# Performance work log

Measured on AMD Instinct MI355X. Metric: run time of the kernel, lower is better.

Reference implementation:

```python
import jax, jax.numpy as jnp
import numpy as np

EPS = 1e-6
BETA = 0.25
NVQ_W = 1.0


def _mlp(h, params):
    # Linear + ReLU on all but last layer (dropout=0, bn=False)
    n = len(params)
    for i, (w, b) in enumerate(params):
        h = h @ w + b
        if i < n - 1:
            h = jax.nn.relu(h)
    return h


def _kuma_ab(a_raw, b_raw):
    return jax.nn.softplus(a_raw) + EPS, jax.nn.softplus(b_raw) + EPS


def _kuma_h(z, a, b):
    x = jnp.clip(jax.nn.sigmoid(z), EPS, 1.0 - EPS)
    inner = jnp.clip(1.0 - x ** a, EPS, 1.0)
    y = 1.0 - inner ** b
    return jnp.clip(y, EPS, 1.0 - EPS)


def _kuma_h_inv(y, a, b):
    y = jnp.clip(y, EPS, 1.0 - EPS)
    omy = jnp.clip(1.0 - y, EPS, 1.0)
    inner = jnp.clip(1.0 - omy ** (1.0 / b), EPS, 1.0 - EPS)
    x = jnp.clip(inner ** (1.0 / a), EPS, 1.0 - EPS)
    return jnp.log(x / (1.0 - x))


def _rq(z, codebooks):
    # Residual VQ: per level, squared-L2 nearest code (argmin), straight-through,
    # codebook + beta*commitment loss. sk_epsilon=0 -> Sinkhorn skipped.
    sg = jax.lax.stop_gradient
    residual = z
    x_q = jnp.zeros_like(z)
    losses, idx_list = [], []
    for l in range(codebooks.shape[0]):
        cb = codebooks[l]  # [K, D]
        d = (jnp.sum(residual * residual, -1, keepdims=True)
             + jnp.sum(cb * cb, -1)
             - 2.0 * residual @ cb.T)  # [B, K]
        idx = jnp.argmin(d, axis=-1)  # [B]
        q = cb[idx]  # [B, D]
        codebook_loss = jnp.mean((q - sg(residual)) ** 2)
        commit_loss = jnp.mean((sg(q) - residual) ** 2)
        losses.append(codebook_loss + BETA * commit_loss)
        q_st = residual + sg(q - residual)  # straight-through
        residual = residual - q_st
        x_q = x_q + q_st
        idx_list.append(idx)
    return x_q, jnp.mean(jnp.stack(losses)), jnp.stack(idx_list, axis=-1)


def _forward(x, enc, dec, codebooks, a_raw, b_raw):
    z = _mlp(x, enc)
    a, b = _kuma_ab(a_raw, b_raw)
    z_prime = _kuma_h(z, a, b)
    zq_prime, rq_loss, indices = _rq(z_prime, codebooks)
    z_q = _kuma_h_inv(zq_prime, a, b)
    z_recon = _kuma_h_inv(z_prime, a, b)
    nvq_loss = jnp.mean((z_recon - z) ** 2)
    total_quant_loss = rq_loss + NVQ_W * nvq_loss
    out = _mlp(z_q, dec)
    return out, total_quant_loss, indices


def setup_inputs() -> dict:
    key = jax.random.key(0)
    ks = jax.random.split(key, 16)
    B, IN = 16384, 768
    enc_dims = [768, 2048, 1024, 512, 128]
    dec_dims = enc_dims[::-1]

    def lin(k, din, dout):
        w = jax.random.normal(k, (din, dout), jnp.float32) * (1.0 / np.sqrt(din))
        return w, jnp.zeros((dout,), jnp.float32)

    inp = {"x": jax.random.normal(ks[0], (B, IN), jnp.float32)}
    for i in range(4):
        w, b = lin(ks[1 + i], enc_dims[i], enc_dims[i + 1])
        inp[f"enc_w{i}"], inp[f"enc_b{i}"] = w, b
        w, b = lin(ks[5 + i], dec_dims[i], dec_dims[i + 1])
        inp[f"dec_w{i}"], inp[f"dec_b{i}"] = w, b
    inp["codebooks"] = jax.random.normal(ks[9], (4, 256, 128), jnp.float32)
    inp["a_raw"] = jnp.zeros((128,), jnp.float32)
    inp["b_raw"] = jnp.zeros((128,), jnp.float32)
    return inp


def reference(x, enc_w0, enc_b0, enc_w1, enc_b1, enc_w2, enc_b2, enc_w3, enc_b3,
              dec_w0, dec_b0, dec_w1, dec_b1, dec_w2, dec_b2, dec_w3, dec_b3,
              codebooks, a_raw, b_raw):
    enc = [(enc_w0, enc_b0), (enc_w1, enc_b1), (enc_w2, enc_b2), (enc_w3, enc_b3)]
    dec = [(dec_w0, dec_b0), (dec_w1, dec_b1), (dec_w2, dec_b2), (dec_w3, dec_b3)]
    return _forward(x, enc, dec, codebooks, a_raw, b_raw)
```

## Files before the change

### kernel.cpp

```cpp
#include <hip/hip_runtime.h>
#include <math.h>

#define EPS_F 1e-6f
#define ONE_M_EPS (1.0f - 1e-6f)

typedef __attribute__((ext_vector_type(8))) short s16x8;
typedef __attribute__((ext_vector_type(8))) _Float16 f16x8;
typedef __attribute__((ext_vector_type(4))) float f32x4;

__device__ __forceinline__ ushort f2bf(float f) {
    union { float f; unsigned u; } v; v.f = f;
    unsigned u = v.u;
    return (ushort)((u + 0x7FFFu + ((u >> 16) & 1u)) >> 16);
}
__device__ __forceinline__ float bf2f(ushort h) {
    union { unsigned u; float f; } v; v.u = ((unsigned)h) << 16;
    return v.f;
}
__device__ __forceinline__ void split2h(float x, ushort& h, ushort& m) {
    union { _Float16 f; ushort u; } a, b;
    a.f = (_Float16)x;
    float r = x - (float)a.f;
    b.f = (_Float16)r;
    h = a.u; m = b.u;
}

#define GLL16(srcp, dstp)                                                     \
    __builtin_amdgcn_global_load_lds(                                         \
        (const __attribute__((address_space(1))) void*)(srcp),                \
        (__attribute__((address_space(3))) void*)(dstp), 16, 0, 0)

__device__ __forceinline__ int swz_k(int row, int k) { return k ^ ((row >> 1) & 3); }

template<bool RELU, int OUT2>
__global__ __launch_bounds__(256) void gemm_mfma_split2(
    const ushort* __restrict__ Ah, const ushort* __restrict__ Am,
    const ushort* __restrict__ Wh, const ushort* __restrict__ Wm,
    const float* __restrict__ bias,
    void* __restrict__ C0, void* __restrict__ C1,
    int M, int N, int K)
{
    __shared__ __align__(16) ushort As[2][128 * 32];
    __shared__ __align__(16) ushort Bs[2][128 * 32];

    const int tid  = threadIdx.x;
    const int lane = tid & 63;
    const int w    = tid >> 6;
    const int wm   = (w >> 1) * 64;
    const int wn   = (w & 1) * 64;
    const int bm   = blockIdx.x * 128;
    const int bn   = blockIdx.y * 128;

    f32x4 acc[4][4];
#pragma unroll
    for (int i = 0; i < 4; i++)
#pragma unroll
        for (int j = 0; j < 4; j++) acc[i][j] = f32x4{0.f, 0.f, 0.f, 0.f};

    const int c0 = (w * 2) * 64 + lane;
    const int c1 = (w * 2 + 1) * 64 + lane;
    const int r0 = c0 >> 2, k0e = swz_k(r0, c0 & 3) * 8;
    const int r1 = c1 >> 2, k1e = swz_k(r1, c1 & 3) * 8;

    const size_t a_off0 = (size_t)(bm + r0) * K + k0e;
    const size_t a_off1 = (size_t)(bm + r1) * K + k1e;
    const size_t b_off0 = (size_t)(bn + r0) * K + k0e;
    const size_t b_off1 = (size_t)(bn + r1) * K + k1e;
    const int d0 = (w * 2) * 512;
    const int d1 = (w * 2 + 1) * 512;

    const ushort* Ap[2] = {Ah, Am};
    const ushort* Wp[2] = {Wh, Wm};

    const int fm  = lane & 15;
    const int fkb = lane >> 4;

    for (int k0 = 0; k0 < K; k0 += 32) {
#pragma unroll
        for (int p = 0; p < 2; p++) {
            GLL16(Ap[p] + a_off0 + k0, &As[p][d0]);
            GLL16(Ap[p] + a_off1 + k0, &As[p][d1]);
            GLL16(Wp[p] + b_off0 + k0, &Bs[p][d0]);
            GLL16(Wp[p] + b_off1 + k0, &Bs[p][d1]);
        }
        __syncthreads();

        f16x8 af[2][4];
#pragma unroll
        for (int p = 0; p < 2; p++)
#pragma unroll
            for (int i = 0; i < 4; i++) {
                const int row = wm + i * 16 + fm;
                af[p][i] = *reinterpret_cast<const f16x8*>(
                    &As[p][row * 32 + swz_k(row, fkb) * 8]);
            }

#pragma unroll
        for (int q = 0; q < 2; q++) {
            f16x8 bq[4];
#pragma unroll
            for (int j = 0; j < 4; j++) {
                const int row = wn + j * 16 + fm;
                bq[j] = *reinterpret_cast<const f16x8*>(
                    &Bs[q][row * 32 + swz_k(row, fkb) * 8]);
            }
#pragma unroll
            for (int p = 0; p < 2; p++) {
                if (p + q <= 1) {
#pragma unroll
                    for (int i = 0; i < 4; i++)
#pragma unroll
                        for (int j = 0; j < 4; j++)
                            acc[i][j] = __builtin_amdgcn_mfma_f32_16x16x32_f16(
                                af[p][i], bq[j], acc[i][j], 0, 0, 0);
                }
            }
        }
        __syncthreads();
    }

#pragma unroll
    for (int j = 0; j < 4; j++) {
        const int coln = bn + wn + j * 16 + fm;
        const float bv = bias[coln];
#pragma unroll
        for (int i = 0; i < 4; i++) {
            const int row0 = bm + wm + i * 16 + (lane >> 4) * 4;
#pragma unroll
            for (int r = 0; r < 4; r++) {
                float o = acc[i][j][r] + bv;
                if (RELU) o = fmaxf(o, 0.f);
                const size_t idx = (size_t)(row0 + r) * N + coln;
                if (OUT2) {
                    ushort h, m;
                    split2h(o, h, m);
                    ((ushort*)C0)[idx] = h;
                    ((ushort*)C1)[idx] = m;
                } else {
                    ((float*)C0)[idx] = o;
                }
            }
        }
    }
}

template<bool RELU, bool OUT_BF16>
__global__ __launch_bounds__(256) void gemm_mfma_bt(
    const ushort* __restrict__ A, const ushort* __restrict__ WT,
    const float* __restrict__ bias, void* __restrict__ Cv,
    int M, int N, int K)
{
    __shared__ __align__(16) ushort As[128 * 32];
    __shared__ __align__(16) ushort Bs[128 * 32];

    const int tid  = threadIdx.x;
    const int lane = tid & 63;
    const int w    = tid >> 6;
    const int wm   = (w >> 1) * 64;
    const int wn   = (w & 1) * 64;
    const int bm   = blockIdx.x * 128;
    const int bn   = blockIdx.y * 128;

    f32x4 acc[4][4];
#pragma unroll
    for (int i = 0; i < 4; i++)
#pragma unroll
        for (int j = 0; j < 4; j++) acc[i][j] = f32x4{0.f, 0.f, 0.f, 0.f};

    const int c0 = (w * 2) * 64 + lane;
    const int c1 = (w * 2 + 1) * 64 + lane;
    const int r0 = c0 >> 2, k0e = swz_k(r0, c0 & 3) * 8;
    const int r1 = c1 >> 2, k1e = swz_k(r1, c1 & 3) * 8;

    const ushort* a_src0 = A  + (size_t)(bm + r0) * K + k0e;
    const ushort* a_src1 = A  + (size_t)(bm + r1) * K + k1e;
    const ushort* b_src0 = WT + (size_t)(bn + r0) * K + k0e;
    const ushort* b_src1 = WT + (size_t)(bn + r1) * K + k1e;
    ushort* a_dst0 = &As[(w * 2) * 512];
    ushort* a_dst1 = &As[(w * 2 + 1) * 512];
    ushort* b_dst0 = &Bs[(w * 2) * 512];
    ushort* b_dst1 = &Bs[(w * 2 + 1) * 512];

    const int fm  = lane & 15;
    const int fkb = lane >> 4;

    for (int k0 = 0; k0 < K; k0 += 32) {
        GLL16(a_src0 + k0, a_dst0);
        GLL16(a_src1 + k0, a_dst1);
        GLL16(b_src0 + k0, b_dst0);
        GLL16(b_src1 + k0, b_dst1);
        __syncthreads();

        s16x8 af[4], bfr[4];
#pragma unroll
        for (int i = 0; i < 4; i++) {
            const int row = wm + i * 16 + fm;
            af[i] = *reinterpret_cast<const s16x8*>(&As[row * 32 + swz_k(row, fkb) * 8]);
        }
#pragma unroll
        for (int j = 0; j < 4; j++) {
            const int row = wn + j * 16 + fm;
            bfr[j] = *reinterpret_cast<const s16x8*>(&Bs[row * 32 + swz_k(row, fkb) * 8]);
        }
#pragma unroll
        for (int i = 0; i < 4; i++)
#pragma unroll
            for (int j = 0; j < 4; j++)
                acc[i][j] = __builtin_amdgcn_mfma_f32_16x16x32_bf16(
                    af[i], bfr[j], acc[i][j], 0, 0, 0);
        __syncthreads();
    }

#pragma unroll
    for (int j = 0; j < 4; j++) {
        const int coln = bn + wn + j * 16 + fm;
        const float bv = bias[coln];
#pragma unroll
        for (int i = 0; i < 4; i++) {
            const int row0 = bm + wm + i * 16 + (lane >> 4) * 4;
#pragma unroll
            for (int r = 0; r < 4; r++) {
                float o = acc[i][j][r] + bv;
                if (RELU) o = fmaxf(o, 0.f);
                if (OUT_BF16)
                    ((ushort*)Cv)[(size_t)(row0 + r) * N + coln] = f2bf(o);
                else
                    ((float*)Cv)[(size_t)(row0 + r) * N + coln] = o;
            }
        }
    }
}

__global__ __launch_bounds__(256) void transpose_to_bf16(
    const float* __restrict__ W, ushort* __restrict__ WT, int K, int N)
{
    __shared__ float t[32][33];
    const int kb = blockIdx.x * 32, nb = blockIdx.y * 32;
    const int tx = threadIdx.x & 31, ty = threadIdx.x >> 5;
#pragma unroll
    for (int i = ty; i < 32; i += 8)
        t[i][tx] = W[(size_t)(kb + i) * N + nb + tx];
    __syncthreads();
#pragma unroll
    for (int i = ty; i < 32; i += 8)
        WT[(size_t)(nb + i) * K + kb + tx] = f2bf(t[tx][i]);
}

__global__ __launch_bounds__(256) void transpose_split_f16(
    const float* __restrict__ W, ushort* __restrict__ TH,
    ushort* __restrict__ TM, int K, int N)
{
    __shared__ float t[32][33];
    const int kb = blockIdx.x * 32, nb = blockIdx.y * 32;
    const int tx = threadIdx.x & 31, ty = threadIdx.x >> 5;
#pragma unroll
    for (int i = ty; i < 32; i += 8)
        t[i][tx] = W[(size_t)(kb + i) * N + nb + tx];
    __syncthreads();
#pragma unroll
    for (int i = ty; i < 32; i += 8) {
        ushort h, m;
        split2h(t[tx][i], h, m);
        const size_t idx = (size_t)(nb + i) * K + kb + tx;
        TH[idx] = h; TM[idx] = m;
    }
}

__global__ __launch_bounds__(256) void split_plane2_kernel(
    const float* __restrict__ X, ushort* __restrict__ H,
    ushort* __restrict__ M, size_t n)
{
    size_t i = (size_t)blockIdx.x * 256 + threadIdx.x;
    if (i >= n) return;
    ushort h, m;
    split2h(X[i], h, m);
    H[i] = h; M[i] = m;
}

__global__ __launch_bounds__(128) void prep_cb_kernel(
    const float* __restrict__ cb, float* __restrict__ cbT, float* __restrict__ cnorm)
{
    int b = blockIdx.x;
    int d = threadIdx.x;
    float v = cb[(size_t)b * 128 + d];
    int l = b >> 8, c = b & 255;
    cbT[((size_t)l * 128 + d) * 256 + c] = v;
    float s = v * v;
#pragma unroll
    for (int off = 32; off > 0; off >>= 1) s += __shfl_down(s, off);
    __shared__ float ps[2];
    if ((d & 63) == 0) ps[d >> 6] = s;
    __syncthreads();
    if (d == 0) cnorm[b] = ps[0] + ps[1];
}

__device__ __forceinline__ float softplusf(float x) {
    return (x > 20.f) ? x : log1pf(expf(x));
}

__global__ void kuma_ab_init(const float* __restrict__ a_raw, const float* __restrict__ b_raw,
                             float* __restrict__ kp)
{
    int t = threadIdx.x;
    if (t < 128) {
        float a = softplusf(a_raw[t]) + EPS_F;
        float b = softplusf(b_raw[t]) + EPS_F;
        kp[t] = a;
        kp[128 + t] = b;
        kp[256 + t] = 1.f / a;
        kp[384 + t] = 1.f / b;
    }
}

__global__ __launch_bounds__(256) void kuma_h_kernel(
    const float* __restrict__ z, const float* __restrict__ kp,
    float* __restrict__ zp, int n)
{
    int i = blockIdx.x * 256 + threadIdx.x;
    if (i >= n) return;
    int col = i & 127;
    float a = kp[col], b = kp[128 + col];
    float zv = z[i];
    float x = 1.f / (1.f + expf(-zv));
    x = fminf(fmaxf(x, EPS_F), ONE_M_EPS);
    float inner = 1.f - powf(x, a);
    inner = fminf(fmaxf(inner, EPS_F), 1.f);
    float y = 1.f - powf(inner, b);
    y = fminf(fmaxf(y, EPS_F), ONE_M_EPS);
    zp[i] = y;
}

__global__ __launch_bounds__(64) void rq_kernel2(
    const float* __restrict__ zp, const float* __restrict__ cb,
    const float* __restrict__ cbT, const float* __restrict__ cnorm,
    float* __restrict__ xq, float* __restrict__ idx_out,
    float* __restrict__ prq, int bid0, int nRq)
{
    __shared__ float res[4][128];

    const int t = threadIdx.x;
    const int row0 = blockIdx.x * 4;

#pragma unroll
    for (int j = 0; j < 8; j++) {
        int e = t + j * 64;
        res[e >> 7][e & 127] = zp[(size_t)row0 * 128 + e];
    }

    float lsum[4];

#pragma unroll 1
    for (int l = 0; l < 4; l++) {
        const float* cT = cbT + (size_t)l * 32768;

        float acc[4][4];
#pragma unroll
        for (int r = 0; r < 4; r++)
#pragma unroll
            for (int cc = 0; cc < 4; cc++) acc[r][cc] = 0.f;

        float pc[16];
#pragma unroll
        for (int dd = 0; dd < 4; dd++)
#pragma unroll
            for (int cc = 0; cc < 4; cc++)
                pc[dd * 4 + cc] = cT[dd * 256 + cc * 64 + t];

#pragma unroll 2
        for (int d = 0; d < 128; d += 4) {
            float nc[16];
            if (d < 124) {
#pragma unroll
                for (int dd = 0; dd < 4; dd++)
#pragma unroll
                    for (int cc = 0; cc < 4; cc++)
                        nc[dd * 4 + cc] = cT[(d + 4 + dd) * 256 + cc * 64 + t];
            }
#pragma unroll
            for (int r = 0; r < 4; r++) {
                float4 rv = *reinterpret_cast<const float4*>(&res[r][d]);
#pragma unroll
                for (int cc = 0; cc < 4; cc++) {
                    acc[r][cc] += rv.x * pc[cc] + rv.y * pc[4 + cc]
                                + rv.z * pc[8 + cc] + rv.w * pc[12 + cc];
                }
            }
#pragma unroll
            for (int k = 0; k < 16; k++) pc[k] = nc[k];
        }

        float cn[4];
#pragma unroll
        for (int cc = 0; cc < 4; cc++) cn[cc] = cnorm[l * 256 + cc * 64 + t];

        int bidx0, bidx1, bidx2, bidx3;
#pragma unroll
        for (int r = 0; r < 4; r++) {
            float dmin = cn[0] - 2.f * acc[r][0];
            int imin = t;
#pragma unroll
            for (int cc = 1; cc < 4; cc++) {
                float dv = cn[cc] - 2.f * acc[r][cc];
                if (dv < dmin) { dmin = dv; imin = cc * 64 + t; }
            }
#pragma unroll
            for (int off = 1; off < 64; off <<= 1) {
                float d2 = __shfl_xor(dmin, off);
                int i2 = __shfl_xor(imin, off);
                if (d2 < dmin || (d2 == dmin && i2 < imin)) { dmin = d2; imin = i2; }
            }
            if (r == 0) bidx0 = imin;
            else if (r == 1) bidx1 = imin;
            else if (r == 2) bidx2 = imin;
            else bidx3 = imin;
            if (t == 0) idx_out[(size_t)(row0 + r) * 4 + l] = (float)imin;
        }

        float s = 0.f;
#pragma unroll
        for (int j = 0; j < 8; j++) {
            const int r = j >> 1;
            const int d = (j & 1) * 64 + t;
            const int bi = (r == 0) ? bidx0 : (r == 1) ? bidx1 : (r == 2) ? bidx2 : bidx3;
            float q = cb[((size_t)(l * 256) + bi) * 128 + d];
            float nr = res[r][d] - q;
            res[r][d] = nr;
            s += nr * nr;
        }
        lsum[l] = s;
    }

#pragma unroll
    for (int j = 0; j < 8; j++) {
        int e = t + j * 64;
        xq[(size_t)row0 * 128 + e] = zp[(size_t)row0 * 128 + e] - res[e >> 7][e & 127];
    }

#pragma unroll
    for (int l = 0; l < 4; l++) {
        float s = lsum[l];
#pragma unroll
        for (int off = 32; off > 0; off >>= 1) s += __shfl_down(s, off);
        if (t == 0) prq[(size_t)l * nRq + bid0 + blockIdx.x] = s;
    }
}

__device__ __forceinline__ float kuma_h_inv_f(float y, float ia, float ib) {
    y = fminf(fmaxf(y, EPS_F), ONE_M_EPS);
    float omy = fminf(fmaxf(1.f - y, EPS_F), 1.f);
    float inner = fminf(fmaxf(1.f - powf(omy, ib), EPS_F), ONE_M_EPS);
    float x = fminf(fmaxf(powf(inner, ia), EPS_F), ONE_M_EPS);
    return logf(x / (1.f - x));
}

__global__ __launch_bounds__(256) void zq_nvq_kernel(
    const float* __restrict__ xq, const float* __restrict__ zp,
    const float* __restrict__ z, const float* __restrict__ kp,
    float* __restrict__ zq, ushort* __restrict__ zq16,
    float* __restrict__ pnvq, int bid0, int n)
{
    int i = blockIdx.x * 256 + threadIdx.x;
    float ds = 0.f;
    if (i < n) {
        int col = i & 127;
        float ia = kp[256 + col], ib = kp[384 + col];
        float xv = xq[i];
        float zpv = zp[i];
        float zv = z[i];
        float zr = kuma_h_inv_f(zpv, ia, ib);
        float d = zr - zv;
        ds = d * d;
        float zqv = kuma_h_inv_f(xv, ia, ib);
        zq[i] = zqv;
        zq16[i] = f2bf(zqv);
    }
#pragma unroll
    for (int off = 32; off > 0; off >>= 1) ds += __shfl_down(ds, off);
    __shared__ float ps[4];
    if ((threadIdx.x & 63) == 0) ps[threadIdx.x >> 6] = ds;
    __syncthreads();
    if (threadIdx.x == 0)
        pnvq[bid0 + blockIdx.x] = ps[0] + ps[1] + ps[2] + ps[3];
}

__global__ __launch_bounds__(256) void finalize_kernel(
    const float* __restrict__ prq, const float* __restrict__ pnvq,
    int nRqAll, int nNvq, float* __restrict__ out_loss)
{
    const int t = threadIdx.x;
    float srq = 0.f, snvq = 0.f;
    for (int i = t; i < nRqAll; i += 256) srq += prq[i];
    for (int i = t; i < nNvq; i += 256) snvq += pnvq[i];
#pragma unroll
    for (int off = 32; off > 0; off >>= 1) {
        srq += __shfl_down(srq, off);
        snvq += __shfl_down(snvq, off);
    }
    __shared__ float pr[4], pn[4];
    if ((t & 63) == 0) { pr[t >> 6] = srq; pn[t >> 6] = snvq; }
    __syncthreads();
    if (t == 0) {
        const float inv = 1.f / (16384.f * 128.f);
        float rq = (pr[0] + pr[1] + pr[2] + pr[3]);
        float nv = (pn[0] + pn[1] + pn[2] + pn[3]);
        out_loss[0] = 0.3125f * rq * inv + nv * inv;
    }
}

extern "C" void kernel_launch(void* const* d_in, const int* in_sizes, int n_in,
                              void* d_out, int out_size, void* d_ws, size_t ws_size,
                              hipStream_t stream)
{
    constexpr int B = 16384;

    const float* x = (const float*)d_in[0];
    const float* enc_w[4]; const float* enc_b[4];
    const float* dec_w[4]; const float* dec_b[4];
    for (int i = 0; i < 4; i++) {
        enc_w[i] = (const float*)d_in[1 + 4 * i];
        enc_b[i] = (const float*)d_in[2 + 4 * i];
        dec_w[i] = (const float*)d_in[3 + 4 * i];
        dec_b[i] = (const float*)d_in[4 + 4 * i];
    }
    const float* cb    = (const float*)d_in[17];
    const float* a_raw = (const float*)d_in[18];
    const float* b_raw = (const float*)d_in[19];

    size_t avail = ws_size / 4;
    const size_t fixed_f = 6547008;
    int R = 16384;
    while (R > 256 && (size_t)R * 3520 + fixed_f > avail) R >>= 1;

    float* ws    = (float*)d_ws;
    float* slotA = ws;
    float* slotB = slotA + (size_t)R * 1024;
    float* zb    = slotB + (size_t)R * 2048;
    float* zpb   = zb  + (size_t)R * 128;
    float* xqb   = zpb + (size_t)R * 128;
    float* zq16f = xqb + (size_t)R * 128;
    float* fixp  = zq16f + (size_t)R * 64;

    ushort* ew = (ushort*)fixp;
    ushort* e0h = ew;            ushort* e0m = e0h + 1572864;
    ushort* e1h = e0m + 1572864; ushort* e1m = e1h + 2097152;
    ushort* e2h = e1m + 2097152; ushort* e2m = e2h + 524288;
    ushort* e3h = e2m + 524288;  ushort* e3m = e3h + 65536;
    ushort* wt0 = e3m + 65536;
    ushort* wt1 = wt0 + 65536;
    ushort* wt2 = wt1 + 524288;
    ushort* wt3 = wt2 + 2097152;
    float* cbT   = (float*)(wt3 + 1572864);
    float* cnorm = cbT + 4 * 128 * 256;
    float* kp    = cnorm + 4 * 256;
    float* prq   = kp + 512;
    float* pnvq  = prq + 16384;

    ushort* zq16 = (ushort*)zq16f;

    ushort* xH  = (ushort*)slotA;  ushort* xM  = xH  + (size_t)R * 768;
    ushort* h0H = (ushort*)slotB;  ushort* h0M = h0H + (size_t)R * 2048;
    ushort* h1H = (ushort*)slotA;  ushort* h1M = h1H + (size_t)R * 1024;
    ushort* h2H = (ushort*)slotB;  ushort* h2M = h2H + (size_t)R * 512;

    ushort* dA = (ushort*)slotB;
    ushort* dB = (ushort*)(slotB + (size_t)R * 256);
    ushort* dC = (ushort*)slotA;

    float* out      = (float*)d_out;
    float* out_loss = out + (size_t)B * 768;
    float* out_idx  = out_loss + 1;

    prep_cb_kernel<<<1024, 128, 0, stream>>>(cb, cbT, cnorm);
    kuma_ab_init<<<1, 128, 0, stream>>>(a_raw, b_raw, kp);
    transpose_split_f16<<<dim3( 768/32, 2048/32), 256, 0, stream>>>(enc_w[0], e0h, e0m,  768, 2048);
    transpose_split_f16<<<dim3(2048/32, 1024/32), 256, 0, stream>>>(enc_w[1], e1h, e1m, 2048, 1024);
    transpose_split_f16<<<dim3(1024/32,  512/32), 256, 0, stream>>>(enc_w[2], e2h, e2m, 1024,  512);
    transpose_split_f16<<<dim3( 512/32,  128/32), 256, 0, stream>>>(enc_w[3], e3h, e3m,  512,  128);
    transpose_to_bf16<<<dim3(128/32,  512/32), 256, 0, stream>>>(dec_w[0], wt0,  128,  512);
    transpose_to_bf16<<<dim3(512/32, 1024/32), 256, 0, stream>>>(dec_w[1], wt1,  512, 1024);
    transpose_to_bf16<<<dim3(1024/32,2048/32), 256, 0, stream>>>(dec_w[2], wt2, 1024, 2048);
    transpose_to_bf16<<<dim3(2048/32, 768/32), 256, 0, stream>>>(dec_w[3], wt3, 2048,  768);

    const int nc = B / R;
    const int nRq = B / 4;
    const int rqPerChunk = R / 4;
    const int nvqPerChunk = (R * 128) / 256;
    for (int c = 0; c < nc; c++) {
        const size_t base = (size_t)c * R;
        const float* xc = x + base * 768;
        float* outc = out + base * 768;
        float* idxc = out_idx + base * 4;

        {
            size_t n = (size_t)R * 768;
            split_plane2_kernel<<<(unsigned)((n + 255) / 256), 256, 0, stream>>>(xc, xH, xM, n);
        }

        gemm_mfma_split2<true , 1><<<dim3(R/128, 16), 256, 0, stream>>>(
            xH, xM, e0h, e0m, enc_b[0], h0H, h0M, R, 2048, 768);
        gemm_mfma_split2<true , 1><<<dim3(R/128,  8), 256, 0, stream>>>(
            h0H, h0M, e1h, e1m, enc_b[1], h1H, h1M, R, 1024, 2048);
        gemm_mfma_split2<true , 1><<<dim3(R/128,  4), 256, 0, stream>>>(
            h1H, h1M, e2h, e2m, enc_b[2], h2H, h2M, R,  512, 1024);
        gemm_mfma_split2<false, 0><<<dim3(R/128,  1), 256, 0, stream>>>(
            h2H, h2M, e3h, e3m, enc_b[3], zb, nullptr, R, 128, 512);

        kuma_h_kernel<<<(R * 128) / 256, 256, 0, stream>>>(zb, kp, zpb, R * 128);
        rq_kernel2<<<rqPerChunk, 64, 0, stream>>>(zpb, cb, cbT, cnorm, xqb, idxc,
                                                  prq, c * rqPerChunk, nRq);
        zq_nvq_kernel<<<nvqPerChunk, 256, 0, stream>>>(xqb, zpb, zb, kp, xqb, zq16,
                                                       pnvq, c * nvqPerChunk, R * 128);

        gemm_mfma_bt<true , true ><<<dim3(R/128,  512/128), 256, 0, stream>>>(zq16, wt0, dec_b[0], dA, R,  512,  128);
        gemm_mfma_bt<true , true ><<<dim3(R/128, 1024/128), 256, 0, stream>>>(dA,   wt1, dec_b[1], dB, R, 1024,  512);
        gemm_mfma_bt<true , true ><<<dim3(R/128, 2048/128), 256, 0, stream>>>(dB,   wt2, dec_b[2], dC, R, 2048, 1024);
        gemm_mfma_bt<false, false><<<dim3(R/128,  768/128), 256, 0, stream>>>(dC,   wt3, dec_b[3], outc, R,  768, 2048);
    }

    finalize_kernel<<<1, 256, 0, stream>>>(prq, pnvq, 4 * nRq, B * 128 / 256, out_loss);
}
```

Baseline: 965.3 us.

## Double-buffer LDS tiles with async prefetch in both MFMA GEMM kernels

Both GEMM kernels now use two LDS stages. The next K-tile is issued via global_load_lds before the current tile is computed, and a partial s_waitcnt vmcnt lets the previous loads complete while new ones stay in flight. MFMA sections are wrapped in s_setprio to favour compute, and the split2 kernel's B-fragment loads and MFMA order are restructured. This doubles LDS use, to 64KB for the split kernel, which may reduce occupancy.

New measurement: 913.5 us, median of 2. 1.06x faster.

```diff
diff --git a/kernel.cpp b/kernel.cpp
--- a/kernel.cpp
+++ b/kernel.cpp
@@ -40,8 +40,8 @@
     void* __restrict__ C0, void* __restrict__ C1,
     int M, int N, int K)
 {
-    __shared__ __align__(16) ushort As[2][128 * 32];
-    __shared__ __align__(16) ushort Bs[2][128 * 32];
+    __shared__ __align__(16) ushort As[2][2][128 * 32];
+    __shared__ __align__(16) ushort Bs[2][2][128 * 32];
 
     const int tid  = threadIdx.x;
     const int lane = tid & 63;
@@ -67,23 +67,40 @@
     const size_t b_off0 = (size_t)(bn + r0) * K + k0e;
     const size_t b_off1 = (size_t)(bn + r1) * K + k1e;
     const int d0 = (w * 2) * 512;
-    const int d1 = (w * 2 + 1) * 512;
+    const int d1 = d0 + 512;
 
     const ushort* Ap[2] = {Ah, Am};
     const ushort* Wp[2] = {Wh, Wm};
 
     const int fm  = lane & 15;
     const int fkb = lane >> 4;
-
-    for (int k0 = 0; k0 < K; k0 += 32) {
-#pragma unroll
-        for (int p = 0; p < 2; p++) {
-            GLL16(Ap[p] + a_off0 + k0, &As[p][d0]);
-            GLL16(Ap[p] + a_off1 + k0, &As[p][d1]);
-            GLL16(Wp[p] + b_off0 + k0, &Bs[p][d0]);
-            GLL16(Wp[p] + b_off1 + k0, &Bs[p][d1]);
-        }
-        __syncthreads();
+    const int NT  = K >> 5;
+
+#pragma unroll
+    for (int p = 0; p < 2; p++) {
+        GLL16(Ap[p] + a_off0, &As[0][p][d0]);
+        GLL16(Ap[p] + a_off1, &As[0][p][d1]);
+        GLL16(Wp[p] + b_off0, &Bs[0][p][d0]);
+        GLL16(Wp[p] + b_off1, &Bs[0][p][d1]);
+    }
+
+    int cur = 0;
+    for (int kt = 0; kt < NT; kt++) {
+        if (kt + 1 < NT) {
+            const int kk = (kt + 1) << 5;
+#pragma unroll
+            for (int p = 0; p < 2; p++) {
+                GLL16(Ap[p] + a_off0 + kk, &As[cur ^ 1][p][d0]);
+                GLL16(Ap[p] + a_off1 + kk, &As[cur ^ 1][p][d1]);
+                GLL16(Wp[p] + b_off0 + kk, &Bs[cur ^ 1][p][d0]);
+                GLL16(Wp[p] + b_off1 + kk, &Bs[cur ^ 1][p][d1]);
+            }
+            asm volatile("s_waitcnt vmcnt(8)" ::: "memory");
+        } else {
+            asm volatile("s_waitcnt vmcnt(0)" ::: "memory");
+        }
+        __builtin_amdgcn_s_barrier();
+        asm volatile("" ::: "memory");
 
         f16x8 af[2][4];
 #pragma unroll
@@ -92,31 +109,29 @@
             for (int i = 0; i < 4; i++) {
                 const int row = wm + i * 16 + fm;
                 af[p][i] = *reinterpret_cast<const f16x8*>(
-                    &As[p][row * 32 + swz_k(row, fkb) * 8]);
-            }
-
-#pragma unroll
-        for (int q = 0; q < 2; q++) {
-            f16x8 bq[4];
+                    &As[cur][p][row * 32 + swz_k(row, fkb) * 8]);
+            }
+        f16x8 bf0[4], bf1[4];
+#pragma unroll
+        for (int j = 0; j < 4; j++) {
+            const int row = wn + j * 16 + fm;
+            bf0[j] = *reinterpret_cast<const f16x8*>(&Bs[cur][0][row * 32 + swz_k(row, fkb) * 8]);
+            bf1[j] = *reinterpret_cast<const f16x8*>(&Bs[cur][1][row * 32 + swz_k(row, fkb) * 8]);
+        }
+
+        __builtin_amdgcn_s_setprio(1);
+#pragma unroll
+        for (int i = 0; i < 4; i++)
 #pragma unroll
             for (int j = 0; j < 4; j++) {
-                const int row = wn + j * 16 + fm;
-                bq[j] = *reinterpret_cast<const f16x8*>(
-                    &Bs[q][row * 32 + swz_k(row, fkb) * 8]);
-            }
-#pragma unroll
-            for (int p = 0; p < 2; p++) {
-                if (p + q <= 1) {
-#pragma unroll
-                    for (int i = 0; i < 4; i++)
-#pragma unroll
-                        for (int j = 0; j < 4; j++)
-                            acc[i][j] = __builtin_amdgcn_mfma_f32_16x16x32_f16(
-                                af[p][i], bq[j], acc[i][j], 0, 0, 0);
-                }
-            }
-        }
-        __syncthreads();
+                acc[i][j] = __builtin_amdgcn_mfma_f32_16x16x32_f16(af[0][i], bf0[j], acc[i][j], 0, 0, 0);
+                acc[i][j] = __builtin_amdgcn_mfma_f32_16x16x32_f16(af[0][i], bf1[j], acc[i][j], 0, 0, 0);
+                acc[i][j] = __builtin_amdgcn_mfma_f32_16x16x32_f16(af[1][i], bf0[j], acc[i][j], 0, 0, 0);
+            }
+        __builtin_amdgcn_s_setprio(0);
+        asm volatile("" ::: "memory");
+        __builtin_amdgcn_s_barrier();
+        cur ^= 1;
     }
 
 #pragma unroll
@@ -150,8 +165,8 @@
     const float* __restrict__ bias, void* __restrict__ Cv,
     int M, int N, int K)
 {
-    __shared__ __align__(16) ushort As[128 * 32];
-    __shared__ __align__(16) ushort Bs[128 * 32];
+    __shared__ __align__(16) ushort As[2][128 * 32];
+    __shared__ __align__(16) ushort Bs[2][128 * 32];
 
     const int tid  = threadIdx.x;
     const int lane = tid & 63;
@@ -176,39 +191,56 @@
     const ushort* a_src1 = A  + (size_t)(bm + r1) * K + k1e;
     const ushort* b_src0 = WT + (size_t)(bn + r0) * K + k0e;
     const ushort* b_src1 = WT + (size_t)(bn + r1) * K + k1e;
-    ushort* a_dst0 = &As[(w * 2) * 512];
-    ushort* a_dst1 = &As[(w * 2 + 1) * 512];
-    ushort* b_dst0 = &Bs[(w * 2) * 512];
-    ushort* b_dst1 = &Bs[(w * 2 + 1) * 512];
+    const int d0 = (w * 2) * 512;
+    const int d1 = d0 + 512;
 
     const int fm  = lane & 15;
     const int fkb = lane >> 4;
-
-    for (int k0 = 0; k0 < K; k0 += 32) {
-        GLL16(a_src0 + k0, a_dst0);
-        GLL16(a_src1 + k0, a_dst1);
-        GLL16(b_src0 + k0, b_dst0);
-        GLL16(b_src1 + k0, b_dst1);
-        __syncthreads();
+    const int NT  = K >> 5;
+
+    GLL16(a_src0, &As[0][d0]);
+    GLL16(a_src1, &As[0][d1]);
+    GLL16(b_src0, &Bs[0][d0]);
+    GLL16(b_src1, &Bs[0][d1]);
+
+    int cur = 0;
+    for (int kt = 0; kt < NT; kt++) {
+        if (kt + 1 < NT) {
+            const int kk = (kt + 1) << 5;
+            GLL16(a_src0 + kk, &As[cur ^ 1][d0]);
+            GLL16(a_src1 + kk, &As[cur ^ 1][d1]);
+            GLL16(b_src0 + kk, &Bs[cur ^ 1][d0]);
+            GLL16(b_src1 + kk, &Bs[cur ^ 1][d1]);
+            asm volatile("s_waitcnt vmcnt(4)" ::: "memory");
+        } else {
+            asm volatile("s_waitcnt vmcnt(0)" ::: "memory");
+        }
+        __builtin_amdgcn_s_barrier();
+        asm volatile("" ::: "memory");
 
         s16x8 af[4], bfr[4];
 #pragma unroll
         for (int i = 0; i < 4; i++) {
             const int row = wm + i * 16 + fm;
-            af[i] = *reinterpret_cast<const s16x8*>(&As[row * 32 + swz_k(row, fkb) * 8]);
+            af[i] = *reinterpret_cast<const s16x8*>(&As[cur][row * 32 + swz_k(row, fkb) * 8]);
         }
 #pragma unroll
         for (int j = 0; j < 4; j++) {
             const int row = wn + j * 16 + fm;
-            bfr[j] = *reinterpret_cast<const s16x8*>(&Bs[row * 32 + swz_k(row, fkb) * 8]);
-        }
+            bfr[j] = *reinterpret_cast<const s16x8*>(&Bs[cur][row * 32 + swz_k(row, fkb) * 8]);
+        }
+
+        __builtin_amdgcn_s_setprio(1);
 #pragma unroll
         for (int i = 0; i < 4; i++)
 #pragma unroll
             for (int j = 0; j < 4; j++)
                 acc[i][j] = __builtin_amdgcn_mfma_f32_16x16x32_bf16(
                     af[i], bfr[j], acc[i][j], 0, 0, 0);
-        __syncthreads();
+        __builtin_amdgcn_s_setprio(0);
+        asm volatile("" ::: "memory");
+        __builtin_amdgcn_s_barrier();
+        cur ^= 1;
     }
 
 #pragma unroll
@@ -611,10 +643,10 @@
         zq_nvq_kernel<<<nvqPerChunk, 256, 0, stream>>>(xqb, zpb, zb, kp, xqb, zq16,
                                                        pnvq, c * nvqPerChunk, R * 128);
 
-        gemm_mfma_bt<true , true ><<<dim3(R/128,  512/128), 256, 0, stream>>>(zq16, wt0, dec_b[0], dA, R,  512,  128);
-        gemm_mfma_bt<true , true ><<<dim3(R/128, 1024/128), 256, 0, stream>>>(dA,   wt1, dec_b[1], dB, R, 1024,  512);
-        gemm_mfma_bt<true , true ><<<dim3(R/128, 2048/128), 256, 0, stream>>>(dB,   wt2, dec_b[2], dC, R, 2048, 1024);
-        gemm_mfma_bt<false, false><<<dim3(R/128,  768/128), 256, 0, stream>>>(dC,   wt3, dec_b[3], outc, R,  768, 2048);
+        gemm_mfma_bt<true , true ><<<dim3(R/128,  4), 256, 0, stream>>>(zq16, wt0, dec_b[0], dA, R,  512,  128);
+        gemm_mfma_bt<true , true ><<<dim3(R/128,  8), 256, 0, stream>>>(dA,   wt1, dec_b[1], dB, R, 1024,  512);
+        gemm_mfma_bt<true , true ><<<dim3(R/128, 16), 256, 0, stream>>>(dB,   wt2, dec_b[2], dC, R, 2048, 1024);
+        gemm_mfma_bt<false, false><<<dim3(R/128,  6), 256, 0, stream>>>(dC,   wt3, dec_b[3], outc, R,  768, 2048);
     }
 
     finalize_kernel<<<1, 256, 0, stream>>>(prq, pnvq, 4 * nRq, B * 128 / 256, out_loss);
```
